# Performance work log

Hardware: AMD Instinct MI355X
Metric: run time of the kernel (lower is better)

## Reference

```python
import jax, jax.numpy as jnp
import numpy as np

H = 8        # num_heads
KNN = 16     # k nearest neighbors
D = 256      # input_dim
LN_EPS = 1e-5


def _make_params(key, D):
    ks = jax.random.split(key, 10)
    def lin(k, din, dout):
        k1, k2 = jax.random.split(k)
        lim = 1.0 / np.sqrt(din)
        W = jax.random.uniform(k1, (din, dout), jnp.float32, -lim, lim)
        b = jax.random.uniform(k2, (dout,), jnp.float32, -lim, lim)
        return W, b
    Wq, bq = lin(ks[0], D, D)
    Wk, bk = lin(ks[1], D, D)
    Wv, bv = lin(ks[2], D, D)
    Wo1, bo1 = lin(ks[3], D, D)
    ln_g = jnp.ones((D,), jnp.float32)
    ln_b = jnp.zeros((D,), jnp.float32)
    Wo2, bo2 = lin(ks[4], D, D)
    return dict(Wq=Wq, bq=bq, Wk=Wk, bk=bk, Wv=Wv, bv=bv,
                Wo1=Wo1, bo1=bo1, ln_g=ln_g, ln_b=ln_b, Wo2=Wo2, bo2=bo2)


def setup_inputs() -> dict:
    key = jax.random.key(0)
    k1, k2, k3, k4, k5 = jax.random.split(key, 5)
    B, N, M = 2, 2048, 4096
    inp = {
        "src": jax.random.normal(k1, (B, N, 3), jnp.float32),
        "tgt": jax.random.normal(k2, (B, M, 3), jnp.float32),
        "src_fea": jax.random.normal(k3, (B, N, D), jnp.float32),
        "tgt_fea": jax.random.normal(k4, (B, M, D), jnp.float32),
    }
    inp.update(_make_params(k5, D))
    return inp


def _cdist(x, y):
    # Euclidean distance [B,N,M], matching torch.cdist(p=2)
    x2 = jnp.sum(x * x, axis=-1, keepdims=True)          # [B,N,1]
    y2 = jnp.sum(y * y, axis=-1, keepdims=True)          # [B,M,1]
    sq = x2 + jnp.swapaxes(y2, -1, -2) - 2.0 * jnp.einsum('bnc,bmc->bnm', x, y)
    return jnp.sqrt(jnp.maximum(sq, 0.0))


def _layernorm(x, g, b):
    mu = jnp.mean(x, axis=-1, keepdims=True)
    var = jnp.mean((x - mu) ** 2, axis=-1, keepdims=True)
    return (x - mu) * jax.lax.rsqrt(var + LN_EPS) * g + b


def reference(src, tgt, src_fea, tgt_fea, Wq, bq, Wk, bk, Wv, bv,
              Wo1, bo1, ln_g, ln_b, Wo2, bo2):
    B, N, Dm = src_fea.shape
    M = tgt.shape[1]
    dk = Dm // H
    scale = dk ** (-0.5)

    # kNN mask: distances [B,N,M], topk smallest -> boolean mask
    dist = _cdist(src, tgt)
    _, knn_idx = jax.lax.top_k(-dist, KNN)               # [B,N,KNN]
    bi = jnp.arange(B)[:, None, None]
    ni = jnp.arange(N)[None, :, None]
    mask = jnp.zeros((B, N, M), bool).at[bi, ni, knn_idx].set(True)

    # projections -> [B,H,*,dk]
    Q = (src_fea @ Wq + bq).reshape(B, N, H, dk).transpose(0, 2, 1, 3)
    K = (tgt_fea @ Wk + bk).reshape(B, M, H, dk).transpose(0, 2, 1, 3)
    V = (tgt_fea @ Wv + bv).reshape(B, M, H, dk).transpose(0, 2, 1, 3)

    scores = jnp.einsum('bhnd,bhmd->bhnm', Q, K) * scale
    scores = jnp.where(mask[:, None], scores, -jnp.inf)
    attn = jax.nn.softmax(scores, axis=-1)               # [B,H,N,M]

    out = jnp.einsum('bhnm,bhmd->bhnd', attn, V)
    out = out.transpose(0, 2, 1, 3).reshape(B, N, Dm)

    x = out + src_fea
    h = jax.nn.relu(_layernorm(x @ Wo1 + bo1, ln_g, ln_b))
    updated = h @ Wo2 + bo2

    avg_attn = jnp.mean(attn, axis=1)                    # [B,N,M]
    return updated, avg_attn
```

## Files before the change

### kernel.cpp

```cpp
#include <hip/hip_runtime.h>
#include <math.h>

#define BB 2
#define NN 2048
#define MM 4096
#define DD 256
#define HH 8
#define DK 32
#define KNN 16

typedef __attribute__((ext_vector_type(8))) short short8;
typedef __attribute__((ext_vector_type(4))) short short4v;
typedef __attribute__((ext_vector_type(4))) float f32x4;
typedef unsigned long long u64;
typedef unsigned short u16;

static __device__ __forceinline__ u16 f2bf(float f) {
    union { float f; unsigned u; } v; v.f = f;
    unsigned r = v.u + 0x7FFF + ((v.u >> 16) & 1);
    return (u16)(r >> 16);
}
static __device__ __forceinline__ float bf2f(u16 u) {
    union { unsigned u; float f; } v; v.u = ((unsigned)u) << 16;
    return v.f;
}

__global__ __launch_bounds__(256)
void wtrans(const float* W0, const float* W1, const float* W2, const float* W3, const float* W4,
            u16* O0, u16* O1, u16* O2, u16* O3, u16* O4)
{
    __shared__ float tile[64][65];
    const int bid = blockIdx.x;
    const int m = bid >> 4, tl = bid & 15;
    const int tr = (tl >> 2) * 64, tc = (tl & 3) * 64;
    const float* W = m == 0 ? W0 : m == 1 ? W1 : m == 2 ? W2 : m == 3 ? W3 : W4;
    u16*        O = m == 0 ? O0 : m == 1 ? O1 : m == 2 ? O2 : m == 3 ? O3 : O4;
    const int c = threadIdx.x & 63, r4 = threadIdx.x >> 6;
    #pragma unroll
    for (int i = 0; i < 16; ++i) {
        const int r = (r4 << 4) + i;
        tile[r][c] = W[(size_t)(tr + r) * 256 + tc + c];
    }
    __syncthreads();
    #pragma unroll
    for (int i = 0; i < 16; ++i) {
        const int cc = (r4 << 4) + i;
        O[(size_t)(tc + cc) * 256 + tr + c] = f2bf(tile[c][cc]);
    }
}

static __device__ __forceinline__ void gemm64_body(
    const float* __restrict__ A, size_t row0, const u16* __restrict__ WT, int col0,
    u16* As, u16* Bs, int t, f32x4 acc[2][2])
{
    const int lane = t & 63, w = t >> 6;
    const int wr = (w >> 1) * 32, wc = (w & 1) * 32;
    for (int k0 = 0; k0 < 256; k0 += 64) {
        #pragma unroll
        for (int e = 0; e < 2; ++e) {
            const int flat = t + (e << 8);
            const int r = flat >> 3, kc = (flat & 7) << 3;
            const int off = ((r << 7) + (kc << 1)) ^ ((r & 7) << 4);
            const float* ap = A + (row0 + r) * 256 + k0 + kc;
            float4 a0 = *(const float4*)ap;
            float4 a1 = *(const float4*)(ap + 4);
            short8 s;
            s[0] = (short)f2bf(a0.x); s[1] = (short)f2bf(a0.y);
            s[2] = (short)f2bf(a0.z); s[3] = (short)f2bf(a0.w);
            s[4] = (short)f2bf(a1.x); s[5] = (short)f2bf(a1.y);
            s[6] = (short)f2bf(a1.z); s[7] = (short)f2bf(a1.w);
            *(short8*)((char*)As + off) = s;
            *(short8*)((char*)Bs + off) = *(const short8*)(WT + (size_t)(col0 + r) * 256 + k0 + kc);
        }
        __syncthreads();
        #pragma unroll
        for (int kk = 0; kk < 64; kk += 32) {
            const int kbo = (kk + ((lane >> 4) << 3)) << 1;
            short8 af[2], bfr[2];
            #pragma unroll
            for (int i = 0; i < 2; ++i) {
                const int ra = wr + (i << 4) + (lane & 15);
                af[i]  = *(const short8*)((const char*)As + (((ra << 7) + kbo) ^ ((ra & 7) << 4)));
                const int rb = wc + (i << 4) + (lane & 15);
                bfr[i] = *(const short8*)((const char*)Bs + (((rb << 7) + kbo) ^ ((rb & 7) << 4)));
            }
            #pragma unroll
            for (int mi = 0; mi < 2; ++mi)
                #pragma unroll
                for (int ni = 0; ni < 2; ++ni)
                    acc[mi][ni] = __builtin_amdgcn_mfma_f32_16x16x32_bf16(af[mi], bfr[ni], acc[mi][ni], 0, 0, 0);
        }
        __syncthreads();
    }
}

__global__ __launch_bounds__(256, 4)
void mega_kernel(const float* __restrict__ src, const float* __restrict__ tgt,
                 int* __restrict__ knn_idx,
                 const float* __restrict__ tgt_fea, const float* __restrict__ src_fea,
                 const u16* __restrict__ WTq, const u16* __restrict__ WTkv,
                 const float* __restrict__ bq, const float* __restrict__ bk,
                 const float* __restrict__ bv,
                 float* __restrict__ Qb, u16* __restrict__ Kbf, u16* __restrict__ Vbf,
                 float* __restrict__ avg)
{
    __shared__ u16 As[64 * 64];
    __shared__ u16 Bs[64 * 64];
    const int bid = blockIdx.x;
    const int t = threadIdx.x;
    const int lane = t & 63;
    const int lid = bid / 11;
    const int role = bid % 11;

    if (role < 4) {
        const int kb = lid * 4 + role;
        const int bn = (kb << 2) + (t >> 6);
        const int b = bn >> 11;
        const float* sp = src + (size_t)bn * 3;
        const float px = sp[0], py = sp[1], pz = sp[2];
        const float x2 = px * px + py * py + pz * pz;
        const float* tb = tgt + (size_t)b * MM * 3;
        unsigned key[64];
        #pragma unroll
        for (int j = 0; j < 64; ++j) {
            const int m = (j << 6) + lane;
            const float tx = tb[m * 3 + 0], ty = tb[m * 3 + 1], tz = tb[m * 3 + 2];
            const float y2 = tx * tx + ty * ty + tz * tz;
            const float dt = px * tx + py * ty + pz * tz;
            float d = (x2 + y2) - 2.0f * dt;
            d = d > 0.f ? d : 0.f;
            const unsigned q20 = (unsigned)fminf(d * 32768.0f, 1048575.0f);
            key[j] = (q20 << 12) | (unsigned)m;
        }
        unsigned last1 = 0;
        unsigned mykey = 0xFFFFFFFFu;
        for (int sel = 0; sel < 20; ++sel) {
            unsigned c0 = ~0u, c1 = ~0u, c2 = ~0u, c3 = ~0u;
            #pragma unroll
            for (int j = 0; j < 64; j += 4) {
                const unsigned u0 = key[j + 0] - last1; c0 = u0 < c0 ? u0 : c0;
                const unsigned u1 = key[j + 1] - last1; c1 = u1 < c1 ? u1 : c1;
                const unsigned u2 = key[j + 2] - last1; c2 = u2 < c2 ? u2 : c2;
                const unsigned u3 = key[j + 3] - last1; c3 = u3 < c3 ? u3 : c3;
            }
            unsigned best = c0 < c1 ? c0 : c1;
            const unsigned bst2 = c2 < c3 ? c2 : c3;
            best = best < bst2 ? best : bst2;
            #pragma unroll
            for (int s = 32; s; s >>= 1) {
                const unsigned o = __shfl_xor(best, s, 64);
                best = o < best ? o : best;
            }
            const unsigned winner = best + last1;
            if (lane == sel) mykey = winner;
            last1 = winner + 1;
        }
        const int midx = (int)(mykey & 0xFFFu);
        u64 ex = ~0ULL;
        if (lane < 20) {
            const float* tp = tb + (size_t)midx * 3;
            const double pxd = px, pyd = py, pzd = pz;
            const double tx = tp[0], ty = tp[1], tz = tp[2];
            const double x2d = pxd * pxd + pyd * pyd + pzd * pzd;
            const double y2d = tx * tx + ty * ty + tz * tz;
            const double dtd = pxd * tx + pyd * ty + pzd * tz;
            double dd = (x2d + y2d) - 2.0 * dtd;
            dd = dd > 0.0 ? dd : 0.0;
            ex = (((u64)__double_as_longlong(dd)) & ~0xFFFULL) | (u64)midx;
        }
        int rank = 0;
        #pragma unroll
        for (int i = 0; i < 20; ++i) {
            const u64 o = __shfl(ex, i, 64);
            rank += (o < ex) ? 1 : 0;
        }
        if (lane < 20 && rank < 16)
            knn_idx[(size_t)bn * KNN + rank] = midx;
        return;
    }

    if (role < 8) {
        const int kvb = lid * 4 + (role - 4);
        const size_t row0 = (size_t)(kvb >> 3) * 64;
        const int col0 = (kvb & 7) * 64;
        f32x4 acc[2][2] = {};
        gemm64_body(tgt_fea, row0, WTkv, col0, As, Bs, t, acc);
        const int w = t >> 6;
        const int wr = (w >> 1) * 32, wc = (w & 1) * 32;
        const bool isv = col0 >= 256;
        u16* ob = isv ? Vbf : Kbf;
        const float* bs = isv ? bv : bk;
        const int cb = (isv ? col0 - 256 : col0) + wc;
        const int cq = lane & 15, rq = (lane >> 4) << 2;
        #pragma unroll
        for (int ni = 0; ni < 2; ++ni) {
            const int c = cb + (ni << 4) + cq;
            const float bval = bs[c];
            #pragma unroll
            for (int mi = 0; mi < 2; ++mi) {
                const size_t r = row0 + wr + (mi << 4) + rq;
                #pragma unroll
                for (int e = 0; e < 4; ++e)
                    ob[(r + e) * 256 + c] = f2bf(acc[mi][ni][e] + bval);
            }
        }
        return;
    }

    if (role == 8) {
        const int qb = lid;
        const size_t row0 = (size_t)(qb >> 2) * 64;
        const int col0 = (qb & 3) * 64;
        f32x4 acc[2][2] = {};
        gemm64_body(src_fea, row0, WTq, col0, As, Bs, t, acc);
        const int w = t >> 6;
        const int wr = (w >> 1) * 32, wc = (w & 1) * 32;
        const int cq = lane & 15, rq = (lane >> 4) << 2;
        #pragma unroll
        for (int ni = 0; ni < 2; ++ni) {
            const int c = col0 + wc + (ni << 4) + cq;
            const float bval = bq[c];
            #pragma unroll
            for (int mi = 0; mi < 2; ++mi) {
                const size_t rbase = (row0 + wr + (mi << 4) + rq) * 256 + c;
                #pragma unroll
                for (int e = 0; e < 4; ++e)
                    Qb[rbase + (size_t)e * 256] = acc[mi][ni][e] + bval;
            }
        }
        return;
    }

    {
        const int zb = lid * 2 + (role - 9);
        f32x4 z = {0.f, 0.f, 0.f, 0.f};
        f32x4* pz = (f32x4*)avg;
        const int base = zb * 256 + t;
        #pragma unroll
        for (int i = 0; i < 32; ++i)
            pz[base + i * 131072] = z;
    }
}

__global__ __launch_bounds__(256)
void attn_kernel(const float* __restrict__ Q, const u16* __restrict__ Kb,
                 const u16* __restrict__ Vb, const int* __restrict__ knn_idx,
                 const float* __restrict__ src_fea,
                 u16* __restrict__ Xb, float* __restrict__ avg_attn)
{
    __shared__ float q_sh[4][256];
    __shared__ float pw_sh[4][8][17];
    __shared__ int   idx_sh[4][16];
    const int t = threadIdx.x;
    const int wid = t >> 6, lane = t & 63;
    const int bn = (blockIdx.x << 2) + wid;
    const int b = bn >> 11;
    const int h = lane >> 3, k2 = lane & 7;

    *(float4*)&q_sh[wid][lane << 2] = *(const float4*)(Q + (size_t)bn * 256 + (lane << 2));
    const int ia = knn_idx[(size_t)bn * KNN + k2];
    const int ib = knn_idx[(size_t)bn * KNN + 8 + k2];
    __syncthreads();

    const u16* Ka = Kb + ((size_t)b * MM + ia) * 256 + h * DK;
    const u16* Kc = Kb + ((size_t)b * MM + ib) * 256 + h * DK;
    const float* qh = &q_sh[wid][h * DK];
    float s0 = 0.f, s1 = 0.f;
    #pragma unroll
    for (int j = 0; j < DK; j += 8) {
        const short8 ka = *(const short8*)(Ka + j);
        const short8 kc = *(const short8*)(Kc + j);
        #pragma unroll
        for (int e = 0; e < 8; ++e) {
            const float qv = qh[j + e];
            s0 = fmaf(qv, bf2f((u16)ka[e]), s0);
            s1 = fmaf(qv, bf2f((u16)kc[e]), s1);
        }
    }
    s0 *= 0.17677669529663688f;
    s1 *= 0.17677669529663688f;

    float m = fmaxf(s0, s1);
    m = fmaxf(m, __shfl_xor(m, 1, 64));
    m = fmaxf(m, __shfl_xor(m, 2, 64));
    m = fmaxf(m, __shfl_xor(m, 4, 64));
    const float e0 = expf(s0 - m), e1 = expf(s1 - m);
    float sum = e0 + e1;
    sum += __shfl_xor(sum, 1, 64);
    sum += __shfl_xor(sum, 2, 64);
    sum += __shfl_xor(sum, 4, 64);
    const float inv = 1.0f / sum;
    const float p0 = e0 * inv, p1 = e1 * inv;

    float a0 = p0, a1 = p1;
    a0 += __shfl_xor(a0, 8, 64);  a1 += __shfl_xor(a1, 8, 64);
    a0 += __shfl_xor(a0, 16, 64); a1 += __shfl_xor(a1, 16, 64);
    a0 += __shfl_xor(a0, 32, 64); a1 += __shfl_xor(a1, 32, 64);
    if (h == 0) {
        avg_attn[(size_t)bn * MM + ia] = a0 * 0.125f;
        avg_attn[(size_t)bn * MM + ib] = a1 * 0.125f;
        idx_sh[wid][k2] = ia;
        idx_sh[wid][8 + k2] = ib;
    }
    pw_sh[wid][h][k2] = p0;
    pw_sh[wid][h][8 + k2] = p1;
    __syncthreads();

    const int d0 = lane << 2;
    const int h2 = lane >> 3;
    float o0 = 0.f, o1 = 0.f, o2 = 0.f, o3 = 0.f;
    #pragma unroll
    for (int k = 0; k < KNN; ++k) {
        const float p = pw_sh[wid][h2][k];
        const int ik = idx_sh[wid][k];
        const short4v v4 = *(const short4v*)(Vb + ((size_t)b * MM + ik) * 256 + d0);
        o0 = fmaf(p, bf2f((u16)v4[0]), o0);
        o1 = fmaf(p, bf2f((u16)v4[1]), o1);
        o2 = fmaf(p, bf2f((u16)v4[2]), o2);
        o3 = fmaf(p, bf2f((u16)v4[3]), o3);
    }
    const float4 sf = *(const float4*)(src_fea + (size_t)bn * 256 + d0);
    short4v xo;
    xo[0] = (short)f2bf(o0 + sf.x);
    xo[1] = (short)f2bf(o1 + sf.y);
    xo[2] = (short)f2bf(o2 + sf.z);
    xo[3] = (short)f2bf(o3 + sf.w);
    *(short4v*)(Xb + (size_t)bn * 256 + d0) = xo;
}

__global__ __launch_bounds__(256)
void gemm_wo1_ln(const u16* __restrict__ A, const u16* __restrict__ WT,
                 const float* __restrict__ bias,
                 const float* __restrict__ g, const float* __restrict__ bvec,
                 u16* __restrict__ outb)
{
    __shared__ u16 As[32 * 64];
    __shared__ u16 Bs[256 * 64];
    const int t = threadIdx.x, lane = t & 63, w = t >> 6;
    const size_t row0 = (size_t)blockIdx.x * 32;
    f32x4 acc[2][4] = {};
    for (int k0 = 0; k0 < 256; k0 += 64) {
        {
            const int r = t >> 3, kc = (t & 7) << 3;
            const int off = ((r << 7) + (kc << 1)) ^ ((r & 7) << 4);
            *(short8*)((char*)As + off) = *(const short8*)(A + (row0 + r) * 256 + k0 + kc);
        }
        #pragma unroll
        for (int e = 0; e < 8; ++e) {
            const int u = t + (e << 8);
            const int r = u >> 3, kc = (u & 7) << 3;
            const int off = ((r << 7) + (kc << 1)) ^ ((r & 7) << 4);
            *(short8*)((char*)Bs + off) = *(const short8*)(WT + (size_t)r * 256 + k0 + kc);
        }
        __syncthreads();
        #pragma unroll
        for (int kk = 0; kk < 64; kk += 32) {
            const int kbo = (kk + ((lane >> 4) << 3)) << 1;
            short8 af[2], bfr[4];
            #pragma unroll
            for (int i = 0; i < 2; ++i) {
                const int ra = (i << 4) + (lane & 15);
                af[i] = *(const short8*)((const char*)As + (((ra << 7) + kbo) ^ ((ra & 7) << 4)));
            }
            #pragma unroll
            for (int i = 0; i < 4; ++i) {
                const int rb = (w << 6) + (i << 4) + (lane & 15);
                bfr[i] = *(const short8*)((const char*)Bs + (((rb << 7) + kbo) ^ ((rb & 7) << 4)));
            }
            #pragma unroll
            for (int mi = 0; mi < 2; ++mi)
                #pragma unroll
                for (int ni = 0; ni < 4; ++ni)
                    acc[mi][ni] = __builtin_amdgcn_mfma_f32_16x16x32_bf16(af[mi], bfr[ni], acc[mi][ni], 0, 0, 0);
        }
        __syncthreads();
    }
    const int cq = lane & 15, rq = (lane >> 4) << 2;
    #pragma unroll
    for (int ni = 0; ni < 4; ++ni) {
        const float bval = bias[(w << 6) + (ni << 4) + cq];
        #pragma unroll
        for (int mi = 0; mi < 2; ++mi)
            #pragma unroll
            for (int e = 0; e < 4; ++e)
                acc[mi][ni][e] += bval;
    }
    float* ws1 = (float*)As;
    float* ws2 = ws1 + 128;
    #pragma unroll
    for (int mi = 0; mi < 2; ++mi)
        #pragma unroll
        for (int e = 0; e < 4; ++e) {
            float s1 = 0.f, s2 = 0.f;
            #pragma unroll
            for (int ni = 0; ni < 4; ++ni) { const float y = acc[mi][ni][e]; s1 += y; s2 += y * y; }
            s1 += __shfl_xor(s1, 1, 64); s2 += __shfl_xor(s2, 1, 64);
            s1 += __shfl_xor(s1, 2, 64); s2 += __shfl_xor(s2, 2, 64);
            s1 += __shfl_xor(s1, 4, 64); s2 += __shfl_xor(s2, 4, 64);
            s1 += __shfl_xor(s1, 8, 64); s2 += __shfl_xor(s2, 8, 64);
            if (cq == 0) {
                const int r = (mi << 4) + rq + e;
                ws1[(w << 5) + r] = s1;
                ws2[(w << 5) + r] = s2;
            }
        }
    __syncthreads();
    float g4[4], b4[4];
    #pragma unroll
    for (int ni = 0; ni < 4; ++ni) {
        const int c = (w << 6) + (ni << 4) + cq;
        g4[ni] = g[c]; b4[ni] = bvec[c];
    }
    #pragma unroll
    for (int mi = 0; mi < 2; ++mi)
        #pragma unroll
        for (int e = 0; e < 4; ++e) {
            const int r = (mi << 4) + rq + e;
            const float s1 = ws1[r] + ws1[32 + r] + ws1[64 + r] + ws1[96 + r];
            const float s2 = ws2[r] + ws2[32 + r] + ws2[64 + r] + ws2[96 + r];
            const float mean = s1 * (1.0f / 256.0f);
            const float var = s2 * (1.0f / 256.0f) - mean * mean;
            const float rstd = 1.0f / sqrtf(var + 1e-5f);
            #pragma unroll
            for (int ni = 0; ni < 4; ++ni) {
                const int c = (w << 6) + (ni << 4) + cq;
                const float y = (acc[mi][ni][e] - mean) * rstd * g4[ni] + b4[ni];
                outb[(row0 + r) * 256 + c] = f2bf(fmaxf(y, 0.0f));
            }
        }
}

__global__ __launch_bounds__(256)
void gemm_wo2(const u16* __restrict__ A, const u16* __restrict__ WT,
              const float* __restrict__ bias, float* __restrict__ outf)
{
    __shared__ u16 As[32 * 64];
    __shared__ u16 Bs[128 * 64];
    const int t = threadIdx.x, lane = t & 63, w = t >> 6;
    const size_t row0 = (size_t)(blockIdx.x >> 1) * 32;
    const int col0 = (blockIdx.x & 1) * 128;
    f32x4 acc[2][2] = {};
    for (int k0 = 0; k0 < 256; k0 += 64) {
        {
            const int r = t >> 3, kc = (t & 7) << 3;
            const int off = ((r << 7) + (kc << 1)) ^ ((r & 7) << 4);
            *(short8*)((char*)As + off) = *(const short8*)(A + (row0 + r) * 256 + k0 + kc);
        }
        #pragma unroll
        for (int e = 0; e < 4; ++e) {
            const int u = t + (e << 8);
            const int r = u >> 3, kc = (u & 7) << 3;
            const int off = ((r << 7) + (kc << 1)) ^ ((r & 7) << 4);
            *(short8*)((char*)Bs + off) = *(const short8*)(WT + (size_t)(col0 + r) * 256 + k0 + kc);
        }
        __syncthreads();
        #pragma unroll
        for (int kk = 0; kk < 64; kk += 32) {
            const int kbo = (kk + ((lane >> 4) << 3)) << 1;
            short8 af[2], bfr[2];
            #pragma unroll
            for (int i = 0; i < 2; ++i) {
                const int ra = (i << 4) + (lane & 15);
                af[i] = *(const short8*)((const char*)As + (((ra << 7) + kbo) ^ ((ra & 7) << 4)));
                const int rb = (w << 5) + (i << 4) + (lane & 15);
                bfr[i] = *(const short8*)((const char*)Bs + (((rb << 7) + kbo) ^ ((rb & 7) << 4)));
            }
            #pragma unroll
            for (int mi = 0; mi < 2; ++mi)
                #pragma unroll
                for (int ni = 0; ni < 2; ++ni)
                    acc[mi][ni] = __builtin_amdgcn_mfma_f32_16x16x32_bf16(af[mi], bfr[ni], acc[mi][ni], 0, 0, 0);
        }
        __syncthreads();
    }
    const int cq = lane & 15, rq = (lane >> 4) << 2;
    #pragma unroll
    for (int ni = 0; ni < 2; ++ni) {
        const int c = col0 + (w << 5) + (ni << 4) + cq;
        const float bval = bias[c];
        #pragma unroll
        for (int mi = 0; mi < 2; ++mi) {
            const size_t rbase = (row0 + (mi << 4) + rq) * 256 + c;
            #pragma unroll
            for (int e = 0; e < 4; ++e)
                outf[rbase + (size_t)e * 256] = acc[mi][ni][e] + bval;
        }
    }
}

extern "C" void kernel_launch(void* const* d_in, const int* in_sizes, int n_in,
                              void* d_out, int out_size, void* d_ws, size_t ws_size,
                              hipStream_t stream) {
    const float* src     = (const float*)d_in[0];
    const float* tgt     = (const float*)d_in[1];
    const float* src_fea = (const float*)d_in[2];
    const float* tgt_fea = (const float*)d_in[3];
    const float* Wq  = (const float*)d_in[4];   const float* bq  = (const float*)d_in[5];
    const float* Wk  = (const float*)d_in[6];   const float* bk  = (const float*)d_in[7];
    const float* Wv  = (const float*)d_in[8];   const float* bv  = (const float*)d_in[9];
    const float* Wo1 = (const float*)d_in[10];  const float* bo1 = (const float*)d_in[11];
    const float* lng = (const float*)d_in[12];  const float* lnb = (const float*)d_in[13];
    const float* Wo2 = (const float*)d_in[14];  const float* bo2 = (const float*)d_in[15];
    (void)in_sizes; (void)n_in; (void)out_size; (void)ws_size;

    float* out     = (float*)d_out;
    float* updated = out;
    float* avg     = out + (size_t)BB * NN * DD;

    char* p = (char*)d_ws;
    u16* WTq  = (u16*)p;   p += 256 * 256 * 2;
    u16* WTk  = (u16*)p;   p += 256 * 256 * 2;
    u16* WTv  = (u16*)p;   p += 256 * 256 * 2;
    u16* WTo1 = (u16*)p;   p += 256 * 256 * 2;
    u16* WTo2 = (u16*)p;   p += 256 * 256 * 2;
    float* Qb = (float*)p; p += (size_t)BB * NN * DD * 4;
    u16* Kbf  = (u16*)p;   p += (size_t)BB * MM * DD * 2;
    u16* Vbf  = (u16*)p;   p += (size_t)BB * MM * DD * 2;
    int* knn  = (int*)p;   p += (size_t)BB * NN * KNN * 4;
    u16* Xbf  = (u16*)p;   p += (size_t)BB * NN * DD * 2;
    u16* Hbf  = (u16*)p;   p += (size_t)BB * NN * DD * 2;

    dim3 blk(256);
    wtrans<<<80, blk, 0, stream>>>(Wq, Wk, Wv, Wo1, Wo2, WTq, WTk, WTv, WTo1, WTo2);
    mega_kernel<<<2816, blk, 0, stream>>>(src, tgt, knn, tgt_fea, src_fea, WTq, WTk,
                                          bq, bk, bv, Qb, Kbf, Vbf, avg);
    attn_kernel<<<BB * NN / 4, blk, 0, stream>>>(Qb, Kbf, Vbf, knn, src_fea, Xbf, avg);
    gemm_wo1_ln<<<BB * NN / 32, blk, 0, stream>>>(Xbf, WTo1, bo1, lng, lnb, Hbf);
    gemm_wo2<<<BB * NN / 16, blk, 0, stream>>>(Hbf, WTo2, bo2, updated);
}
```

Baseline: 183.7 us.

## Stream kNN selection with per-lane top-4 and fuse attention with output MLP

```diff
diff --git a/kernel.cpp b/kernel.cpp
--- a/kernel.cpp
+++ b/kernel.cpp
@@ -94,6 +94,24 @@
     }
 }
 
+static __device__ __forceinline__ unsigned refill_min(
+    const float* __restrict__ tb, int lane, float px, float py, float pz,
+    float x2, unsigned last)
+{
+    unsigned best = 0xFFFFFFFFu;
+    #pragma unroll 1
+    for (int j = 0; j < 64; ++j) {
+        const int m = (j << 6) + lane;
+        const float tx = tb[m*3+0], ty = tb[m*3+1], tz = tb[m*3+2];
+        const float y2 = tx*tx + ty*ty + tz*tz;
+        float d = (x2 + y2) - 2.0f*(px*tx + py*ty + pz*tz);
+        d = d > 0.f ? d : 0.f;
+        const unsigned k = ((unsigned)fminf(d*32768.f, 1048574.f) << 12) | (unsigned)m;
+        if (k > last && k < best) best = k;
+    }
+    return best;
+}
+
 __global__ __launch_bounds__(256, 4)
 void mega_kernel(const float* __restrict__ src, const float* __restrict__ tgt,
                  int* __restrict__ knn_idx,
@@ -109,78 +127,102 @@
     const int bid = blockIdx.x;
     const int t = threadIdx.x;
     const int lane = t & 63;
-    const int lid = bid / 11;
-    const int role = bid % 11;
-
-    if (role < 4) {
-        const int kb = lid * 4 + role;
-        const int bn = (kb << 2) + (t >> 6);
-        const int b = bn >> 11;
-        const float* sp = src + (size_t)bn * 3;
-        const float px = sp[0], py = sp[1], pz = sp[2];
-        const float x2 = px * px + py * py + pz * pz;
+    const int lid = bid / 9;
+    const int role = bid % 9;
+
+    if (role < 2) {
+        const int kb = lid * 2 + role;
+        const int wid = t >> 6;
+        const int bn0 = (kb << 3) + (wid << 1);
+        const int b = bn0 >> 11;
+        const float* spA = src + (size_t)bn0 * 3;
+        const float pxA = spA[0], pyA = spA[1], pzA = spA[2];
+        const float pxB = spA[3], pyB = spA[4], pzB = spA[5];
+        const float x2A = pxA*pxA + pyA*pyA + pzA*pzA;
+        const float x2B = pxB*pxB + pyB*pyB + pzB*pzB;
         const float* tb = tgt + (size_t)b * MM * 3;
-        unsigned key[64];
-        #pragma unroll
+        unsigned sA0=~0u,sA1=~0u,sA2=~0u,sA3=~0u;
+        unsigned sB0=~0u,sB1=~0u,sB2=~0u,sB3=~0u;
+        #pragma unroll 8
         for (int j = 0; j < 64; ++j) {
             const int m = (j << 6) + lane;
-            const float tx = tb[m * 3 + 0], ty = tb[m * 3 + 1], tz = tb[m * 3 + 2];
-            const float y2 = tx * tx + ty * ty + tz * tz;
-            const float dt = px * tx + py * ty + pz * tz;
-            float d = (x2 + y2) - 2.0f * dt;
-            d = d > 0.f ? d : 0.f;
-            const unsigned q20 = (unsigned)fminf(d * 32768.0f, 1048575.0f);
-            key[j] = (q20 << 12) | (unsigned)m;
-        }
-        unsigned last1 = 0;
-        unsigned mykey = 0xFFFFFFFFu;
+            const float tx = tb[m*3+0], ty = tb[m*3+1], tz = tb[m*3+2];
+            const float y2 = tx*tx + ty*ty + tz*tz;
+            float dA = (x2A + y2) - 2.0f*(pxA*tx + pyA*ty + pzA*tz);
+            float dB = (x2B + y2) - 2.0f*(pxB*tx + pyB*ty + pzB*tz);
+            dA = dA > 0.f ? dA : 0.f;
+            dB = dB > 0.f ? dB : 0.f;
+            const unsigned kA = ((unsigned)fminf(dA*32768.f, 1048574.f) << 12) | (unsigned)m;
+            const unsigned kB = ((unsigned)fminf(dB*32768.f, 1048574.f) << 12) | (unsigned)m;
+            if (kA < sA3) {
+                sA3 = kA; unsigned tt;
+                tt=sA2; sA2=tt<sA3?tt:sA3; sA3=tt<sA3?sA3:tt;
+                tt=sA1; sA1=tt<sA2?tt:sA2; sA2=tt<sA2?sA2:tt;
+                tt=sA0; sA0=tt<sA1?tt:sA1; sA1=tt<sA1?sA1:tt;
+            }
+            if (kB < sB3) {
+                sB3 = kB; unsigned tt;
+                tt=sB2; sB2=tt<sB3?tt:sB3; sB3=tt<sB3?sB3:tt;
+                tt=sB1; sB1=tt<sB2?tt:sB2; sB2=tt<sB2?sB2:tt;
+                tt=sB0; sB0=tt<sB1?tt:sB1; sB1=tt<sB1?sB1:tt;
+            }
+        }
+        unsigned lastA = 0, lastB = 0, myA = 0, myB = 0;
         for (int sel = 0; sel < 20; ++sel) {
-            unsigned c0 = ~0u, c1 = ~0u, c2 = ~0u, c3 = ~0u;
-            #pragma unroll
-            for (int j = 0; j < 64; j += 4) {
-                const unsigned u0 = key[j + 0] - last1; c0 = u0 < c0 ? u0 : c0;
-                const unsigned u1 = key[j + 1] - last1; c1 = u1 < c1 ? u1 : c1;
-                const unsigned u2 = key[j + 2] - last1; c2 = u2 < c2 ? u2 : c2;
-                const unsigned u3 = key[j + 3] - last1; c3 = u3 < c3 ? u3 : c3;
-            }
-            unsigned best = c0 < c1 ? c0 : c1;
-            const unsigned bst2 = c2 < c3 ? c2 : c3;
-            best = best < bst2 ? best : bst2;
-            #pragma unroll
-            for (int s = 32; s; s >>= 1) {
-                const unsigned o = __shfl_xor(best, s, 64);
-                best = o < best ? o : best;
-            }
-            const unsigned winner = best + last1;
-            if (lane == sel) mykey = winner;
-            last1 = winner + 1;
-        }
-        const int midx = (int)(mykey & 0xFFFu);
-        u64 ex = ~0ULL;
+            if (__any(sA0 == 0xFFFFFFFFu)) {
+                if (sA0 == 0xFFFFFFFFu) sA0 = refill_min(tb, lane, pxA,pyA,pzA, x2A, lastA);
+            }
+            if (__any(sB0 == 0xFFFFFFFFu)) {
+                if (sB0 == 0xFFFFFFFFu) sB0 = refill_min(tb, lane, pxB,pyB,pzB, x2B, lastB);
+            }
+            unsigned wA = sA0, wB = sB0;
+            #pragma unroll
+            for (int s2 = 1; s2 <= 32; s2 <<= 1) {
+                const unsigned oA = __shfl_xor(wA, s2, 64); wA = oA < wA ? oA : wA;
+                const unsigned oB = __shfl_xor(wB, s2, 64); wB = oB < wB ? oB : wB;
+            }
+            if (lane == sel) { myA = wA; myB = wB; }
+            if (sA0 == wA) { lastA = sA0; sA0=sA1; sA1=sA2; sA2=sA3; sA3=0xFFFFFFFFu; }
+            if (sB0 == wB) { lastB = sB0; sB0=sB1; sB1=sB2; sB2=sB3; sB3=0xFFFFFFFFu; }
+        }
+        const int midxA = (int)(myA & 0xFFFu);
+        const int midxB = (int)(myB & 0xFFFu);
+        u64 exA = ~0ULL, exB = ~0ULL;
         if (lane < 20) {
-            const float* tp = tb + (size_t)midx * 3;
-            const double pxd = px, pyd = py, pzd = pz;
-            const double tx = tp[0], ty = tp[1], tz = tp[2];
-            const double x2d = pxd * pxd + pyd * pyd + pzd * pzd;
-            const double y2d = tx * tx + ty * ty + tz * tz;
-            const double dtd = pxd * tx + pyd * ty + pzd * tz;
-            double dd = (x2d + y2d) - 2.0 * dtd;
-            dd = dd > 0.0 ? dd : 0.0;
-            ex = (((u64)__double_as_longlong(dd)) & ~0xFFFULL) | (u64)midx;
-        }
-        int rank = 0;
+            {
+                const float* tp = tb + (size_t)midxA * 3;
+                const double pxd = pxA, pyd = pyA, pzd = pzA;
+                const double tx = tp[0], ty = tp[1], tz = tp[2];
+                const double x2d = pxd*pxd + pyd*pyd + pzd*pzd;
+                const double y2d = tx*tx + ty*ty + tz*tz;
+                double dd = (x2d + y2d) - 2.0*(pxd*tx + pyd*ty + pzd*tz);
+                dd = dd > 0.0 ? dd : 0.0;
+                exA = (((u64)__double_as_longlong(dd)) & ~0xFFFULL) | (u64)midxA;
+            }
+            {
+                const float* tp = tb + (size_t)midxB * 3;
+                const double pxd = pxB, pyd = pyB, pzd = pzB;
+                const double tx = tp[0], ty = tp[1], tz = tp[2];
+                const double x2d = pxd*pxd + pyd*pyd + pzd*pzd;
+                const double y2d = tx*tx + ty*ty + tz*tz;
+                double dd = (x2d + y2d) - 2.0*(pxd*tx + pyd*ty + pzd*tz);
+                dd = dd > 0.0 ? dd : 0.0;
+                exB = (((u64)__double_as_longlong(dd)) & ~0xFFFULL) | (u64)midxB;
+            }
+        }
+        int rankA = 0, rankB = 0;
         #pragma unroll
         for (int i = 0; i < 20; ++i) {
-            const u64 o = __shfl(ex, i, 64);
-            rank += (o < ex) ? 1 : 0;
-        }
-        if (lane < 20 && rank < 16)
-            knn_idx[(size_t)bn * KNN + rank] = midx;
+            rankA += (__shfl(exA, i, 64) < exA) ? 1 : 0;
+            rankB += (__shfl(exB, i, 64) < exB) ? 1 : 0;
+        }
+        if (lane < 20 && rankA < 16) knn_idx[(size_t)bn0 * KNN + rankA] = midxA;
+        if (lane < 20 && rankB < 16) knn_idx[((size_t)bn0 + 1) * KNN + rankB] = midxB;
         return;
     }
 
-    if (role < 8) {
-        const int kvb = lid * 4 + (role - 4);
+    if (role < 6) {
+        const int kvb = lid * 4 + (role - 2);
         const size_t row0 = (size_t)(kvb >> 3) * 64;
         const int col0 = (kvb & 7) * 64;
         f32x4 acc[2][2] = {};
@@ -207,7 +249,7 @@
         return;
     }
 
-    if (role == 8) {
+    if (role == 6) {
         const int qb = lid;
         const size_t row0 = (size_t)(qb >> 2) * 64;
         const int col0 = (qb & 3) * 64;
@@ -232,7 +274,7 @@
     }
 
     {
-        const int zb = lid * 2 + (role - 9);
+        const int zb = lid * 2 + (role - 7);
         f32x4 z = {0.f, 0.f, 0.f, 0.f};
         f32x4* pz = (f32x4*)avg;
         const int base = zb * 256 + t;
@@ -242,18 +284,25 @@
     }
 }
 
-__global__ __launch_bounds__(256)
-void attn_kernel(const float* __restrict__ Q, const u16* __restrict__ Kb,
+__global__ __launch_bounds__(1024)
+void tail_kernel(const float* __restrict__ Q, const u16* __restrict__ Kb,
                  const u16* __restrict__ Vb, const int* __restrict__ knn_idx,
                  const float* __restrict__ src_fea,
-                 u16* __restrict__ Xb, float* __restrict__ avg_attn)
+                 const u16* __restrict__ WTo1, const float* __restrict__ bo1,
+                 const float* __restrict__ lng, const float* __restrict__ lnb,
+                 const u16* __restrict__ WTo2, const float* __restrict__ bo2,
+                 float* __restrict__ updated, float* __restrict__ avg_attn)
 {
-    __shared__ float q_sh[4][256];
-    __shared__ float pw_sh[4][8][17];
-    __shared__ int   idx_sh[4][16];
+    __shared__ float q_sh[16][256];
+    __shared__ float pw_sh[16][8][17];
+    __shared__ int   idx_sh[16][16];
+    __shared__ u16   Xs[16 * 256];
+    __shared__ u16   Hs[16 * 256];
+    __shared__ float2 red2[16][16];
     const int t = threadIdx.x;
     const int wid = t >> 6, lane = t & 63;
-    const int bn = (blockIdx.x << 2) + wid;
+    const int r0 = blockIdx.x << 4;
+    const int bn = r0 + wid;
     const int b = bn >> 11;
     const int h = lane >> 3, k2 = lane & 7;
 
@@ -280,11 +329,11 @@
     s0 *= 0.17677669529663688f;
     s1 *= 0.17677669529663688f;
 
-    float m = fmaxf(s0, s1);
-    m = fmaxf(m, __shfl_xor(m, 1, 64));
-    m = fmaxf(m, __shfl_xor(m, 2, 64));
-    m = fmaxf(m, __shfl_xor(m, 4, 64));
-    const float e0 = expf(s0 - m), e1 = expf(s1 - m);
+    float mx = fmaxf(s0, s1);
+    mx = fmaxf(mx, __shfl_xor(mx, 1, 64));
+    mx = fmaxf(mx, __shfl_xor(mx, 2, 64));
+    mx = fmaxf(mx, __shfl_xor(mx, 4, 64));
+    const float e0 = expf(s0 - mx), e1 = expf(s1 - mx);
     float sum = e0 + e1;
     sum += __shfl_xor(sum, 1, 64);
     sum += __shfl_xor(sum, 2, 64);
@@ -306,184 +355,101 @@
     pw_sh[wid][h][8 + k2] = p1;
     __syncthreads();
 
-    const int d0 = lane << 2;
-    const int h2 = lane >> 3;
-    float o0 = 0.f, o1 = 0.f, o2 = 0.f, o3 = 0.f;
+    {
+        const int d0 = lane << 2;
+        const int h2 = lane >> 3;
+        float o0 = 0.f, o1 = 0.f, o2 = 0.f, o3 = 0.f;
+        #pragma unroll
+        for (int k = 0; k < KNN; ++k) {
+            const float p = pw_sh[wid][h2][k];
+            const int ik = idx_sh[wid][k];
+            const short4v v4 = *(const short4v*)(Vb + ((size_t)b * MM + ik) * 256 + d0);
+            o0 = fmaf(p, bf2f((u16)v4[0]), o0);
+            o1 = fmaf(p, bf2f((u16)v4[1]), o1);
+            o2 = fmaf(p, bf2f((u16)v4[2]), o2);
+            o3 = fmaf(p, bf2f((u16)v4[3]), o3);
+        }
+        const float4 sf = *(const float4*)(src_fea + (size_t)bn * 256 + d0);
+        short4v xo;
+        xo[0] = (short)f2bf(o0 + sf.x);
+        xo[1] = (short)f2bf(o1 + sf.y);
+        xo[2] = (short)f2bf(o2 + sf.z);
+        xo[3] = (short)f2bf(o3 + sf.w);
+        const int off = ((wid << 9) + (d0 << 1)) ^ ((wid & 7) << 4);
+        *(short4v*)((char*)Xs + off) = xo;
+    }
+    __syncthreads();
+
+    const int cq = lane & 15, ks = lane >> 4;
+    const int colB = (wid << 4) + cq;
+    f32x4 acc = {};
     #pragma unroll
-    for (int k = 0; k < KNN; ++k) {
-        const float p = pw_sh[wid][h2][k];
-        const int ik = idx_sh[wid][k];
-        const short4v v4 = *(const short4v*)(Vb + ((size_t)b * MM + ik) * 256 + d0);
-        o0 = fmaf(p, bf2f((u16)v4[0]), o0);
-        o1 = fmaf(p, bf2f((u16)v4[1]), o1);
-        o2 = fmaf(p, bf2f((u16)v4[2]), o2);
-        o3 = fmaf(p, bf2f((u16)v4[3]), o3);
-    }
-    const float4 sf = *(const float4*)(src_fea + (size_t)bn * 256 + d0);
-    short4v xo;
-    xo[0] = (short)f2bf(o0 + sf.x);
-    xo[1] = (short)f2bf(o1 + sf.y);
-    xo[2] = (short)f2bf(o2 + sf.z);
-    xo[3] = (short)f2bf(o3 + sf.w);
-    *(short4v*)(Xb + (size_t)bn * 256 + d0) = xo;
-}
-
-__global__ __launch_bounds__(256)
-void gemm_wo1_ln(const u16* __restrict__ A, const u16* __restrict__ WT,
-                 const float* __restrict__ bias,
-                 const float* __restrict__ g, const float* __restrict__ bvec,
-                 u16* __restrict__ outb)
-{
-    __shared__ u16 As[32 * 64];
-    __shared__ u16 Bs[256 * 64];
-    const int t = threadIdx.x, lane = t & 63, w = t >> 6;
-    const size_t row0 = (size_t)blockIdx.x * 32;
-    f32x4 acc[2][4] = {};
-    for (int k0 = 0; k0 < 256; k0 += 64) {
-        {
-            const int r = t >> 3, kc = (t & 7) << 3;
-            const int off = ((r << 7) + (kc << 1)) ^ ((r & 7) << 4);
-            *(short8*)((char*)As + off) = *(const short8*)(A + (row0 + r) * 256 + k0 + kc);
-        }
-        #pragma unroll
-        for (int e = 0; e < 8; ++e) {
-            const int u = t + (e << 8);
-            const int r = u >> 3, kc = (u & 7) << 3;
-            const int off = ((r << 7) + (kc << 1)) ^ ((r & 7) << 4);
-            *(short8*)((char*)Bs + off) = *(const short8*)(WT + (size_t)r * 256 + k0 + kc);
-        }
-        __syncthreads();
-        #pragma unroll
-        for (int kk = 0; kk < 64; kk += 32) {
-            const int kbo = (kk + ((lane >> 4) << 3)) << 1;
-            short8 af[2], bfr[4];
-            #pragma unroll
-            for (int i = 0; i < 2; ++i) {
-                const int ra = (i << 4) + (lane & 15);
-                af[i] = *(const short8*)((const char*)As + (((ra << 7) + kbo) ^ ((ra & 7) << 4)));
-            }
-            #pragma unroll
-            for (int i = 0; i < 4; ++i) {
-                const int rb = (w << 6) + (i << 4) + (lane & 15);
-                bfr[i] = *(const short8*)((const char*)Bs + (((rb << 7) + kbo) ^ ((rb & 7) << 4)));
-            }
-            #pragma unroll
-            for (int mi = 0; mi < 2; ++mi)
-                #pragma unroll
-                for (int ni = 0; ni < 4; ++ni)
-                    acc[mi][ni] = __builtin_amdgcn_mfma_f32_16x16x32_bf16(af[mi], bfr[ni], acc[mi][ni], 0, 0, 0);
-        }
-        __syncthreads();
-    }
-    const int cq = lane & 15, rq = (lane >> 4) << 2;
+    for (int kk = 0; kk < 256; kk += 32) {
+        const int k8 = kk + (ks << 3);
+        const short8 af = *(const short8*)((const char*)Xs + (((cq << 9) + (k8 << 1)) ^ ((cq & 7) << 4)));
+        const short8 bfrg = *(const short8*)(WTo1 + (size_t)colB * 256 + k8);
+        acc = __builtin_amdgcn_mfma_f32_16x16x32_bf16(af, bfrg, acc, 0, 0, 0);
+    }
+    {
+        const float bval = bo1[colB];
+        #pragma unroll
+        for (int e = 0; e < 4; ++e) acc[e] += bval;
+    }
+    {
+        float s1v[4], s2v[4];
+        #pragma unroll
+        for (int e = 0; e < 4; ++e) {
+            float v = acc[e], vv = acc[e] * acc[e];
+            v += __shfl_xor(v, 1, 64); vv += __shfl_xor(vv, 1, 64);
+            v += __shfl_xor(v, 2, 64); vv += __shfl_xor(vv, 2, 64);
+            v += __shfl_xor(v, 4, 64); vv += __shfl_xor(vv, 4, 64);
+            v += __shfl_xor(v, 8, 64); vv += __shfl_xor(vv, 8, 64);
+            s1v[e] = v; s2v[e] = vv;
+        }
+        if (cq == 0) {
+            #pragma unroll
+            for (int e = 0; e < 4; ++e) {
+                float2 pr; pr.x = s1v[e]; pr.y = s2v[e];
+                red2[wid][(ks << 2) + e] = pr;
+            }
+        }
+    }
+    __syncthreads();
+    {
+        const float gv = lng[colB], bv = lnb[colB];
+        #pragma unroll
+        for (int e = 0; e < 4; ++e) {
+            const int r = (ks << 2) + e;
+            float S1 = 0.f, S2 = 0.f;
+            #pragma unroll
+            for (int w2 = 0; w2 < 16; ++w2) {
+                const float2 pr = red2[w2][r];
+                S1 += pr.x; S2 += pr.y;
+            }
+            const float mean = S1 * (1.0f / 256.0f);
+            const float var = S2 * (1.0f / 256.0f) - mean * mean;
+            const float rstd = 1.0f / sqrtf(var + 1e-5f);
+            const float y = (acc[e] - mean) * rstd * gv + bv;
+            const int off = ((r << 9) + (colB << 1)) ^ ((r & 7) << 4);
+            *(u16*)((char*)Hs + off) = f2bf(fmaxf(y, 0.0f));
+        }
+    }
+    __syncthreads();
+
+    f32x4 acc2 = {};
     #pragma unroll
-    for (int ni = 0; ni < 4; ++ni) {
-        const float bval = bias[(w << 6) + (ni << 4) + cq];
-        #pragma unroll
-        for (int mi = 0; mi < 2; ++mi)
-            #pragma unroll
-            for (int e = 0; e < 4; ++e)
-                acc[mi][ni][e] += bval;
-    }
-    float* ws1 = (float*)As;
-    float* ws2 = ws1 + 128;
-    #pragma unroll
-    for (int mi = 0; mi < 2; ++mi)
+    for (int kk = 0; kk < 256; kk += 32) {
+        const int k8 = kk + (ks << 3);
+        const short8 af = *(const short8*)((const char*)Hs + (((cq << 9) + (k8 << 1)) ^ ((cq & 7) << 4)));
+        const short8 bfrg = *(const short8*)(WTo2 + (size_t)colB * 256 + k8);
+        acc2 = __builtin_amdgcn_mfma_f32_16x16x32_bf16(af, bfrg, acc2, 0, 0, 0);
+    }
+    {
+        const float bval = bo2[colB];
         #pragma unroll
         for (int e = 0; e < 4; ++e) {
-            float s1 = 0.f, s2 = 0.f;
-            #pragma unroll
-            for (int ni = 0; ni < 4; ++ni) { const float y = acc[mi][ni][e]; s1 += y; s2 += y * y; }
-            s1 += __shfl_xor(s1, 1, 64); s2 += __shfl_xor(s2, 1, 64);
-            s1 += __shfl_xor(s1, 2, 64); s2 += __shfl_xor(s2, 2, 64);
-            s1 += __shfl_xor(s1, 4, 64); s2 += __shfl_xor(s2, 4, 64);
-            s1 += __shfl_xor(s1, 8, 64); s2 += __shfl_xor(s2, 8, 64);
-            if (cq == 0) {
-                const int r = (mi << 4) + rq + e;
-                ws1[(w << 5) + r] = s1;
-                ws2[(w << 5) + r] = s2;
-            }
-        }
-    __syncthreads();
-    float g4[4], b4[4];
-    #pragma unroll
-    for (int ni = 0; ni < 4; ++ni) {
-        const int c = (w << 6) + (ni << 4) + cq;
-        g4[ni] = g[c]; b4[ni] = bvec[c];
-    }
-    #pragma unroll
-    for (int mi = 0; mi < 2; ++mi)
-        #pragma unroll
-        for (int e = 0; e < 4; ++e) {
-            const int r = (mi << 4) + rq + e;
-            const float s1 = ws1[r] + ws1[32 + r] + ws1[64 + r] + ws1[96 + r];
-            const float s2 = ws2[r] + ws2[32 + r] + ws2[64 + r] + ws2[96 + r];
-            const float mean = s1 * (1.0f / 256.0f);
-            const float var = s2 * (1.0f / 256.0f) - mean * mean;
-            const float rstd = 1.0f / sqrtf(var + 1e-5f);
-            #pragma unroll
-            for (int ni = 0; ni < 4; ++ni) {
-                const int c = (w << 6) + (ni << 4) + cq;
-                const float y = (acc[mi][ni][e] - mean) * rstd * g4[ni] + b4[ni];
-                outb[(row0 + r) * 256 + c] = f2bf(fmaxf(y, 0.0f));
-            }
-        }
-}
-
-__global__ __launch_bounds__(256)
-void gemm_wo2(const u16* __restrict__ A, const u16* __restrict__ WT,
-              const float* __restrict__ bias, float* __restrict__ outf)
-{
-    __shared__ u16 As[32 * 64];
-    __shared__ u16 Bs[128 * 64];
-    const int t = threadIdx.x, lane = t & 63, w = t >> 6;
-    const size_t row0 = (size_t)(blockIdx.x >> 1) * 32;
-    const int col0 = (blockIdx.x & 1) * 128;
-    f32x4 acc[2][2] = {};
-    for (int k0 = 0; k0 < 256; k0 += 64) {
-        {
-            const int r = t >> 3, kc = (t & 7) << 3;
-            const int off = ((r << 7) + (kc << 1)) ^ ((r & 7) << 4);
-            *(short8*)((char*)As + off) = *(const short8*)(A + (row0 + r) * 256 + k0 + kc);
-        }
-        #pragma unroll
-        for (int e = 0; e < 4; ++e) {
-            const int u = t + (e << 8);
-            const int r = u >> 3, kc = (u & 7) << 3;
-            const int off = ((r << 7) + (kc << 1)) ^ ((r & 7) << 4);
-            *(short8*)((char*)Bs + off) = *(const short8*)(WT + (size_t)(col0 + r) * 256 + k0 + kc);
-        }
-        __syncthreads();
-        #pragma unroll
-        for (int kk = 0; kk < 64; kk += 32) {
-            const int kbo = (kk + ((lane >> 4) << 3)) << 1;
-            short8 af[2], bfr[2];
-            #pragma unroll
-            for (int i = 0; i < 2; ++i) {
-                const int ra = (i << 4) + (lane & 15);
-                af[i] = *(const short8*)((const char*)As + (((ra << 7) + kbo) ^ ((ra & 7) << 4)));
-                const int rb = (w << 5) + (i << 4) + (lane & 15);
-                bfr[i] = *(const short8*)((const char*)Bs + (((rb << 7) + kbo) ^ ((rb & 7) << 4)));
-            }
-            #pragma unroll
-            for (int mi = 0; mi < 2; ++mi)
-                #pragma unroll
-                for (int ni = 0; ni < 2; ++ni)
-                    acc[mi][ni] = __builtin_amdgcn_mfma_f32_16x16x32_bf16(af[mi], bfr[ni], acc[mi][ni], 0, 0, 0);
-        }
-        __syncthreads();
-    }
-    const int cq = lane & 15, rq = (lane >> 4) << 2;
-    #pragma unroll
-    for (int ni = 0; ni < 2; ++ni) {
-        const int c = col0 + (w << 5) + (ni << 4) + cq;
-        const float bval = bias[c];
-        #pragma unroll
-        for (int mi = 0; mi < 2; ++mi) {
-            const size_t rbase = (row0 + (mi << 4) + rq) * 256 + c;
-            #pragma unroll
-            for (int e = 0; e < 4; ++e)
-                outf[rbase + (size_t)e * 256] = acc[mi][ni][e] + bval;
+            const int r = (ks << 2) + e;
+            updated[(size_t)(r0 + r) * 256 + colB] = acc2[e] + bval;
         }
     }
 }
@@ -517,14 +483,12 @@
     u16* Kbf  = (u16*)p;   p += (size_t)BB * MM * DD * 2;
     u16* Vbf  = (u16*)p;   p += (size_t)BB * MM * DD * 2;
     int* knn  = (int*)p;   p += (size_t)BB * NN * KNN * 4;
-    u16* Xbf  = (u16*)p;   p += (size_t)BB * NN * DD * 2;
-    u16* Hbf  = (u16*)p;   p += (size_t)BB * NN * DD * 2;
 
     dim3 blk(256);
     wtrans<<<80, blk, 0, stream>>>(Wq, Wk, Wv, Wo1, Wo2, WTq, WTk, WTv, WTo1, WTo2);
-    mega_kernel<<<2816, blk, 0, stream>>>(src, tgt, knn, tgt_fea, src_fea, WTq, WTk,
+    mega_kernel<<<2304, blk, 0, stream>>>(src, tgt, knn, tgt_fea, src_fea, WTq, WTk,
                                           bq, bk, bv, Qb, Kbf, Vbf, avg);
-    attn_kernel<<<BB * NN / 4, blk, 0, stream>>>(Qb, Kbf, Vbf, knn, src_fea, Xbf, avg);
-    gemm_wo1_ln<<<BB * NN / 32, blk, 0, stream>>>(Xbf, WTo1, bo1, lng, lnb, Hbf);
-    gemm_wo2<<<BB * NN / 16, blk, 0, stream>>>(Hbf, WTo2, bo2, updated);
-}
+    tail_kernel<<<256, dim3(1024), 0, stream>>>(Qb, Kbf, Vbf, knn, src_fea,
+                                                WTo1, bo1, lng, lnb, WTo2, bo2,
+                                                updated, avg);
+}
```

Measured after the change: 191.1 us. +4.0%, slower.
